# Kernel tuning notes

Measured on AMD Instinct MI355X. Metric: run time of the kernel, lower is better.

The kernel has to match this reference:

```python
import jax, jax.numpy as jnp
import numpy as np

BURN_MIN, BURN_MAX = 0.2, 0.8
B, C, H, W, S = 32, 3, 512, 512, 8  # S = num_spots (fixed at max of original 3..8)


def setup_inputs() -> dict:
    key = jax.random.key(0)
    k1, k2, k3, k4, k5 = jax.random.split(key, 5)
    return {
        "img": jax.random.uniform(k1, (B, C, H, W), dtype=jnp.float32),
        "u_xy": jax.random.uniform(k2, (B, S, 2), dtype=jnp.float32),
        "u_radius": jax.random.uniform(k3, (B, S), dtype=jnp.float32),
        "u_intensity": jax.random.uniform(k4, (B, S), dtype=jnp.float32),
        "u_burn": jax.random.uniform(k5, (B,), dtype=jnp.float32),
    }


def reference(img, u_xy, u_radius, u_intensity, u_burn):
    dtype = img.dtype
    # coordinate grid in [-1, 1]
    y = jnp.linspace(-1.0, 1.0, H, dtype=dtype)
    x = jnp.linspace(-1.0, 1.0, W, dtype=dtype)
    yc, xc = jnp.meshgrid(y, x, indexing="ij")  # [H, W]

    # edge weight (shared across batch)
    dist = jnp.sqrt(xc ** 2 + yc ** 2)
    ew = jnp.exp(2.0 * (dist - 0.7))
    ew = (ew - ew.min()) / (ew.max() - ew.min() + 1e-6)  # [H, W]

    # map uniforms to the original random ranges
    spot_xy = 2.0 * u_xy - 1.0                     # [B, S, 2] in [-1, 1]
    radius = 0.05 + 0.15 * u_radius                # [B, S] in [0.05, 0.2]
    sint = 0.5 + 0.5 * u_intensity                 # [B, S] in [0.5, 1.0]
    burn = BURN_MIN + (BURN_MAX - BURN_MIN) * u_burn  # [B]

    sx = spot_xy[..., 0][:, :, None, None]         # [B, S, 1, 1]
    sy = spot_xy[..., 1][:, :, None, None]
    # squared distance to spot centers: [B, S, H, W]
    d2 = (xc[None, None] - sx) ** 2 + (yc[None, None] - sy) ** 2
    spot_mask = jnp.exp(-d2 / (2.0 * radius[:, :, None, None] ** 2)) * sint[:, :, None, None]
    spots = spot_mask.max(axis=1)                  # [B, H, W]

    burn_mask = jnp.clip(jnp.maximum(ew[None], spots) * burn[:, None, None], 0.0, 1.0)
    bm = burn_mask[:, None]                        # [B, 1, H, W]

    dark_scale = jnp.array([0.7, 0.4, 0.3], dtype=dtype)[None, :, None, None]
    darkening = img * dark_scale
    out = jnp.clip(img * (1.0 - bm) + darkening * bm, 0.0, 1.0)
    return out
```

## Files before the change

### kernel.cpp

```cpp
#include <hip/hip_runtime.h>
#include <math.h>


namespace {
constexpr int B = 32, C = 3, H = 512, W = 512, S = 8;
constexpr int PLANE = H * W;
constexpr int BLOCKS_PER_BATCH = PLANE / 4 / 256;
constexpr float LOG2E = 1.4426950408889634f;
typedef float fvec4 __attribute__((ext_vector_type(4)));
}

__global__ __launch_bounds__(256) void pizza_burn_kernel(
    const float* __restrict__ img,
    const float* __restrict__ u_xy,
    const float* __restrict__ u_radius,
    const float* __restrict__ u_intensity,
    const float* __restrict__ u_burn,
    float* __restrict__ out,
    const float ew_scale, const float ew_bias)
{
  const int b    = blockIdx.x >> 8;
  const int pix4 = ((blockIdx.x & 255) << 8) | threadIdx.x;
  const int h    = pix4 >> 7;
  const int w0   = (pix4 & 127) << 2;

  const float delta = 2.0f / 511.0f;
  const float yc = fmaf((float)h, delta, -1.0f);
  const float y2 = yc * yc;

  const float* uxy = u_xy        + (size_t)b * S * 2;
  const float* urd = u_radius    + (size_t)b * S;
  const float* uin = u_intensity + (size_t)b * S;
  float sx[S], sy[S], nc[S], lsi[S];
#pragma unroll
  for (int s = 0; s < S; ++s) {
    sx[s] = fmaf(2.0f, uxy[2 * s + 0], -1.0f);
    sy[s] = fmaf(2.0f, uxy[2 * s + 1], -1.0f);
    const float r = fmaf(0.15f, urd[s], 0.05f);
    nc[s]  = -LOG2E / (2.0f * r * r);
    lsi[s] = __builtin_amdgcn_logf(fmaf(0.5f, uin[s], 0.5f));
  }
  const float burn = fmaf(0.6f, u_burn[b], 0.2f);

  float bm[4];
#pragma unroll
  for (int j = 0; j < 4; ++j) {
    const float xc   = fmaf((float)(w0 + j), delta, -1.0f);
    const float dist = __builtin_amdgcn_sqrtf(fmaf(xc, xc, y2));
    const float ew   = __builtin_amdgcn_exp2f(fmaf(dist, 2.0f * LOG2E, -1.4f * LOG2E));
    const float ewn  = fmaf(ew, ew_scale, ew_bias);
    float lm = -3.0e38f;
#pragma unroll
    for (int s = 0; s < S; ++s) {
      const float dx = xc - sx[s];
      const float dy = yc - sy[s];
      const float d2 = fmaf(dx, dx, dy * dy);
      lm = fmaxf(lm, fmaf(d2, nc[s], lsi[s]));
    }
    const float spots = __builtin_amdgcn_exp2f(lm);
    bm[j] = fminf(fmaxf(fmaxf(ewn, spots) * burn, 0.0f), 1.0f);
  }

  const float omds[3] = {1.0f - 0.7f, 1.0f - 0.4f, 1.0f - 0.3f};
  const size_t base = (size_t)b * (C * PLANE) + (size_t)h * W + w0;
#pragma unroll
  for (int c = 0; c < C; ++c) {
    const fvec4 v = *reinterpret_cast<const fvec4*>(img + base + (size_t)c * PLANE);
    fvec4 o;
    const float k = omds[c];
    o.x = fminf(fmaxf(v.x * fmaf(-bm[0], k, 1.0f), 0.0f), 1.0f);
    o.y = fminf(fmaxf(v.y * fmaf(-bm[1], k, 1.0f), 0.0f), 1.0f);
    o.z = fminf(fmaxf(v.z * fmaf(-bm[2], k, 1.0f), 0.0f), 1.0f);
    o.w = fminf(fmaxf(v.w * fmaf(-bm[3], k, 1.0f), 0.0f), 1.0f);
    __builtin_nontemporal_store(o, reinterpret_cast<fvec4*>(out + base + (size_t)c * PLANE));
  }
}

extern "C" void kernel_launch(void* const* d_in, const int* in_sizes, int n_in,
                              void* d_out, int out_size, void* d_ws, size_t ws_size,
                              hipStream_t stream) {
  const float* img         = (const float*)d_in[0];
  const float* u_xy        = (const float*)d_in[1];
  const float* u_radius    = (const float*)d_in[2];
  const float* u_intensity = (const float*)d_in[3];
  const float* u_burn      = (const float*)d_in[4];
  float* out = (float*)d_out;

  const float delta = 2.0f / 511.0f;
  const float cmin  = fabsf(-1.0f + 255.0f * delta);
  const float dmin  = sqrtf(2.0f * cmin * cmin);
  const float dmax  = sqrtf(2.0f);
  const float ew_min = expf(2.0f * (dmin - 0.7f));
  const float ew_max = expf(2.0f * (dmax - 0.7f));
  const float inv_range = 1.0f / (ew_max - ew_min + 1e-6f);
  const float ew_bias = -ew_min * inv_range;

  dim3 grid(B * BLOCKS_PER_BATCH);
  dim3 block(256);
  pizza_burn_kernel<<<grid, block, 0, stream>>>(img, u_xy, u_radius, u_intensity,
                                                u_burn, out, inv_range, ew_bias);
}
```

Baseline: 180.6 us.

## Process eight pixels per thread, issue image loads early, hoist per-row spot terms

Each thread now handles eight pixels instead of four, halving the grid. All six image vector loads are issued before the spot math so memory latency overlaps the mask computation. The y-dependent part of each spot's Gaussian is precomputed once per row, using a reciprocal intrinsic in place of division. Stores switch from nontemporal to regular, and the larger per-thread footprint raises register use and cuts the number of waves available to hide latency.

```diff
diff --git a/kernel.cpp b/kernel.cpp
--- a/kernel.cpp
+++ b/kernel.cpp
@@ -5,7 +5,8 @@
 namespace {
 constexpr int B = 32, C = 3, H = 512, W = 512, S = 8;
 constexpr int PLANE = H * W;
-constexpr int BLOCKS_PER_BATCH = PLANE / 4 / 256;
+constexpr int PIX8_PER_BATCH = PLANE / 8;
+constexpr int BLOCKS_PER_BATCH = PIX8_PER_BATCH / 256;
 constexpr float LOG2E = 1.4426950408889634f;
 typedef float fvec4 __attribute__((ext_vector_type(4)));
 }
@@ -19,10 +20,18 @@
     float* __restrict__ out,
     const float ew_scale, const float ew_bias)
 {
-  const int b    = blockIdx.x >> 8;
-  const int pix4 = ((blockIdx.x & 255) << 8) | threadIdx.x;
-  const int h    = pix4 >> 7;
-  const int w0   = (pix4 & 127) << 2;
+  const int b    = blockIdx.x >> 7;
+  const int pix8 = ((blockIdx.x & 127) << 8) | threadIdx.x;
+  const int h    = pix8 >> 6;
+  const int w0   = (pix8 & 63) << 3;
+
+  const size_t base = (size_t)b * (C * PLANE) + (size_t)h * W + w0;
+  fvec4 v[6];
+#pragma unroll
+  for (int c = 0; c < C; ++c) {
+    v[2 * c + 0] = *reinterpret_cast<const fvec4*>(img + base + (size_t)c * PLANE);
+    v[2 * c + 1] = *reinterpret_cast<const fvec4*>(img + base + (size_t)c * PLANE + 4);
+  }
 
   const float delta = 2.0f / 511.0f;
   const float yc = fmaf((float)h, delta, -1.0f);
@@ -31,20 +40,22 @@
   const float* uxy = u_xy        + (size_t)b * S * 2;
   const float* urd = u_radius    + (size_t)b * S;
   const float* uin = u_intensity + (size_t)b * S;
-  float sx[S], sy[S], nc[S], lsi[S];
+  float sx[S], nc[S], cy[S];
 #pragma unroll
   for (int s = 0; s < S; ++s) {
     sx[s] = fmaf(2.0f, uxy[2 * s + 0], -1.0f);
-    sy[s] = fmaf(2.0f, uxy[2 * s + 1], -1.0f);
-    const float r = fmaf(0.15f, urd[s], 0.05f);
-    nc[s]  = -LOG2E / (2.0f * r * r);
-    lsi[s] = __builtin_amdgcn_logf(fmaf(0.5f, uin[s], 0.5f));
+    const float sy = fmaf(2.0f, uxy[2 * s + 1], -1.0f);
+    const float r  = fmaf(0.15f, urd[s], 0.05f);
+    nc[s] = (-0.5f * LOG2E) * __builtin_amdgcn_rcpf(r * r);
+    const float lsi = __builtin_amdgcn_logf(fmaf(0.5f, uin[s], 0.5f));
+    const float dy  = yc - sy;
+    cy[s] = fmaf(nc[s] * dy, dy, lsi);
   }
   const float burn = fmaf(0.6f, u_burn[b], 0.2f);
 
-  float bm[4];
+  float bm[8];
 #pragma unroll
-  for (int j = 0; j < 4; ++j) {
+  for (int j = 0; j < 8; ++j) {
     const float xc   = fmaf((float)(w0 + j), delta, -1.0f);
     const float dist = __builtin_amdgcn_sqrtf(fmaf(xc, xc, y2));
     const float ew   = __builtin_amdgcn_exp2f(fmaf(dist, 2.0f * LOG2E, -1.4f * LOG2E));
@@ -52,27 +63,28 @@
     float lm = -3.0e38f;
 #pragma unroll
     for (int s = 0; s < S; ++s) {
-      const float dx = xc - sx[s];
-      const float dy = yc - sy[s];
-      const float d2 = fmaf(dx, dx, dy * dy);
-      lm = fmaxf(lm, fmaf(d2, nc[s], lsi[s]));
+      const float t = xc - sx[s];
+      lm = fmaxf(lm, fmaf(nc[s] * t, t, cy[s]));
     }
     const float spots = __builtin_amdgcn_exp2f(lm);
     bm[j] = fminf(fmaxf(fmaxf(ewn, spots) * burn, 0.0f), 1.0f);
   }
 
   const float omds[3] = {1.0f - 0.7f, 1.0f - 0.4f, 1.0f - 0.3f};
-  const size_t base = (size_t)b * (C * PLANE) + (size_t)h * W + w0;
 #pragma unroll
   for (int c = 0; c < C; ++c) {
-    const fvec4 v = *reinterpret_cast<const fvec4*>(img + base + (size_t)c * PLANE);
-    fvec4 o;
     const float k = omds[c];
-    o.x = fminf(fmaxf(v.x * fmaf(-bm[0], k, 1.0f), 0.0f), 1.0f);
-    o.y = fminf(fmaxf(v.y * fmaf(-bm[1], k, 1.0f), 0.0f), 1.0f);
-    o.z = fminf(fmaxf(v.z * fmaf(-bm[2], k, 1.0f), 0.0f), 1.0f);
-    o.w = fminf(fmaxf(v.w * fmaf(-bm[3], k, 1.0f), 0.0f), 1.0f);
-    __builtin_nontemporal_store(o, reinterpret_cast<fvec4*>(out + base + (size_t)c * PLANE));
+    fvec4 o0, o1;
+    o0.x = fminf(fmaxf(v[2*c].x   * fmaf(-bm[0], k, 1.0f), 0.0f), 1.0f);
+    o0.y = fminf(fmaxf(v[2*c].y   * fmaf(-bm[1], k, 1.0f), 0.0f), 1.0f);
+    o0.z = fminf(fmaxf(v[2*c].z   * fmaf(-bm[2], k, 1.0f), 0.0f), 1.0f);
+    o0.w = fminf(fmaxf(v[2*c].w   * fmaf(-bm[3], k, 1.0f), 0.0f), 1.0f);
+    o1.x = fminf(fmaxf(v[2*c+1].x * fmaf(-bm[4], k, 1.0f), 0.0f), 1.0f);
+    o1.y = fminf(fmaxf(v[2*c+1].y * fmaf(-bm[5], k, 1.0f), 0.0f), 1.0f);
+    o1.z = fminf(fmaxf(v[2*c+1].z * fmaf(-bm[6], k, 1.0f), 0.0f), 1.0f);
+    o1.w = fminf(fmaxf(v[2*c+1].w * fmaf(-bm[7], k, 1.0f), 0.0f), 1.0f);
+    *reinterpret_cast<fvec4*>(out + base + (size_t)c * PLANE)     = o0;
+    *reinterpret_cast<fvec4*>(out + base + (size_t)c * PLANE + 4) = o1;
   }
 }
 
```

Measured after the change: 181.1 us. About the same (+0.3%).
